# Performance work log

Measured on AMD Instinct MI355X. Metric: run time of the kernel, lower is better.

Reference implementation:

```python
import jax, jax.numpy as jnp
import numpy as np
from jax import lax

# Mamba-2 block, mode='recurrent' (chunked SSD scan), default vanilla causal dwconv
D_MODEL = 2048
D_STATE = 64
D_CONV = 4
HEADDIM = 64
EXPAND = 2
NGROUPS = 1
CHUNK = 64
D_INNER = EXPAND * D_MODEL          # 4096
NHEADS = D_INNER // HEADDIM          # 64
CONV_DIM = D_INNER + 2 * NGROUPS * D_STATE   # 4224
D_IN_PROJ = 2 * D_INNER + 2 * NGROUPS * D_STATE + NHEADS  # 8384
BATCH, SEQ = 2, 4096
EPS = 1e-5


def setup_inputs() -> dict:
    key = jax.random.key(0)
    ks = jax.random.split(key, 8)
    x = jax.random.normal(ks[0], (BATCH, SEQ, D_MODEL), jnp.float32)
    in_proj_w = jax.random.normal(ks[1], (D_IN_PROJ, D_MODEL), jnp.float32) / np.sqrt(D_MODEL)
    conv_w = jax.random.normal(ks[2], (CONV_DIM, D_CONV), jnp.float32) / np.sqrt(D_CONV)
    conv_b = jnp.zeros((CONV_DIM,), jnp.float32)
    # dt_bias = inverse-softplus of dt sampled log-uniform in [1e-3, 1e-1]
    dt = jnp.exp(jax.random.uniform(ks[3], (NHEADS,)) * (np.log(0.1) - np.log(0.001)) + np.log(0.001))
    dt_bias = dt + jnp.log(-jnp.expm1(-dt))
    A_log = jnp.log(jax.random.uniform(ks[4], (NHEADS,), minval=1.0, maxval=16.0))
    D = jnp.ones((NHEADS,), jnp.float32)
    norm_w = jnp.ones((D_INNER,), jnp.float32)
    out_proj_w = jax.random.normal(ks[5], (D_MODEL, D_INNER), jnp.float32) / np.sqrt(D_INNER)
    return dict(x=x, in_proj_w=in_proj_w, conv_w=conv_w, conv_b=conv_b,
                dt_bias=dt_bias, A_log=A_log, D=D, norm_w=norm_w, out_proj_w=out_proj_w)


def _segsum(a):
    """a: (..., T) -> (..., T, T) lower-triangular segment sums."""
    T = a.shape[-1]
    cs = jnp.cumsum(a, axis=-1)
    d = cs[..., :, None] - cs[..., None, :]
    mask = jnp.tril(jnp.ones((T, T), dtype=bool))
    return jnp.where(mask, d, -jnp.inf)


def _forward(x, in_proj_w, conv_w, conv_b, dt_bias, A_log, D, norm_w, out_proj_w):
    Bsz, L, _ = x.shape
    nc = L // CHUNK
    zxbcdt = x @ in_proj_w.T                      # (B,L,D_IN_PROJ)
    z = zxbcdt[..., :D_INNER]
    xBC = zxbcdt[..., D_INNER:D_INNER + CONV_DIM]
    dt = zxbcdt[..., D_INNER + CONV_DIM:]         # (B,L,H)

    # causal depthwise conv1d (padding = d_conv-1, sliced to L) + SiLU
    xBC_t = jnp.transpose(xBC, (0, 2, 1))         # (B,C,L)
    y = lax.conv_general_dilated(xBC_t, conv_w[:, None, :], window_strides=(1,),
                                 padding=[(D_CONV - 1, 0)],
                                 feature_group_count=CONV_DIM,
                                 dimension_numbers=('NCH', 'OIH', 'NCH'))
    y = y + conv_b[None, :, None]
    xBC = jax.nn.silu(jnp.transpose(y, (0, 2, 1)))  # (B,L,C)

    xs = xBC[..., :D_INNER]
    Bm = xBC[..., D_INNER:D_INNER + NGROUPS * D_STATE]
    Cm = xBC[..., D_INNER + NGROUPS * D_STATE:]

    dt = jax.nn.softplus(dt + dt_bias)            # (B,L,H)
    A = -jnp.exp(A_log)                           # (H,)
    dA = dt * A                                   # (B,L,H)

    xh = xs.reshape(Bsz, L, NHEADS, HEADDIM)
    Bh = jnp.repeat(Bm.reshape(Bsz, L, NGROUPS, D_STATE), NHEADS // NGROUPS, axis=2)  # (B,L,H,N)
    Ch = jnp.repeat(Cm.reshape(Bsz, L, NGROUPS, D_STATE), NHEADS // NGROUPS, axis=2)
    xdt = xh * dt[..., None]                      # (B,L,H,P)

    # chunk
    Ac = dA.reshape(Bsz, nc, CHUNK, NHEADS).transpose(0, 1, 3, 2)  # (B,c,H,l)
    A_cumsum = jnp.cumsum(Ac, axis=-1)                             # (B,c,H,l)
    Lmat = jnp.exp(_segsum(Ac))                                    # (B,c,H,l,s)
    Cc = Ch.reshape(Bsz, nc, CHUNK, NHEADS, D_STATE)
    Bc = Bh.reshape(Bsz, nc, CHUNK, NHEADS, D_STATE)
    xc = xdt.reshape(Bsz, nc, CHUNK, NHEADS, HEADDIM)

    # intra-chunk (diagonal blocks)
    Y_diag = jnp.einsum('bclhn,bcshn,bchls,bcshp->bclhp', Cc, Bc, Lmat, xc)

    # per-chunk end states
    decay_states = jnp.exp(A_cumsum[..., -1:] - A_cumsum)          # (B,c,H,l)
    states = jnp.einsum('bcshn,bchs,bcshp->bchpn', Bc, decay_states, xc)  # (B,c,H,P,N)
    chunk_decay = jnp.exp(A_cumsum[..., -1])                       # (B,c,H)

    # inter-chunk recurrence over chunks
    def scan_fn(h, inp):
        dec, st = inp                              # (B,H), (B,H,P,N)
        prev = h
        h = dec[..., None, None] * h + st
        return h, prev

    h0 = jnp.zeros((Bsz, NHEADS, HEADDIM, D_STATE), x.dtype)
    _, prev_states = lax.scan(scan_fn, h0,
                              (chunk_decay.transpose(1, 0, 2), states.transpose(1, 0, 2, 3, 4)))
    prev_states = prev_states.transpose(1, 0, 2, 3, 4)             # (B,c,H,P,N)

    Y_off = jnp.einsum('bclhn,bchpn,bchl->bclhp', Cc, prev_states, jnp.exp(A_cumsum))

    Y = (Y_diag + Y_off).reshape(Bsz, L, NHEADS, HEADDIM) + D[:, None] * xh
    yf = Y.reshape(Bsz, L, D_INNER)

    # gated RMSNorm, then out projection
    yf = yf * jax.nn.silu(z)
    yf = yf * lax.rsqrt(jnp.mean(yf * yf, axis=-1, keepdims=True) + EPS) * norm_w
    return yf @ out_proj_w.T


def reference(x, in_proj_w, conv_w, conv_b, dt_bias, A_log, D, norm_w, out_proj_w):
    return _forward(x, in_proj_w, conv_w, conv_b, dt_bias, A_log, D, norm_w, out_proj_w)
```

## Files before the change

kernel.cpp:

```cpp
#include <hip/hip_runtime.h>

#define BATCH 2
#define SEQ 4096
#define DMODEL 2048
#define DINNER 4096
#define NHEADS 64
#define HEADDIM 64
#define DSTATE 64
#define CONVDIM 4224
#define DINPROJ 8384
#define NCHUNK 64
#define CHUNKL 64
#define MROWS (BATCH*SEQ)

typedef __bf16 bf16_t;
typedef bf16_t bf16x8 __attribute__((ext_vector_type(8)));
typedef float f32x4 __attribute__((ext_vector_type(4)));
typedef unsigned short u16;
typedef u16 u16x8 __attribute__((ext_vector_type(8)));

__device__ __forceinline__ u16 f2bf(float f) {
  unsigned int u = __float_as_uint(f);
  u += 0x7fff + ((u >> 16) & 1);
  return (u16)(u >> 16);
}
__device__ __forceinline__ float bf2f(u16 s) {
  return __uint_as_float(((unsigned int)s) << 16);
}

__device__ __forceinline__ void async_load16(const void* g, void* l) {
  __builtin_amdgcn_global_load_lds(
      (const __attribute__((address_space(1))) void*)g,
      (__attribute__((address_space(3))) void*)l, 16, 0, 0);
}

__global__ __launch_bounds__(256) void cvt_kernel(const float* __restrict__ in,
                                                  u16* __restrict__ out, int n4) {
  int i = blockIdx.x * 256 + threadIdx.x;
  if (i >= n4) return;
  float4 v = *(const float4*)(in + (size_t)i * 4);
  ushort4 o;
  o.x = f2bf(v.x); o.y = f2bf(v.y); o.z = f2bf(v.z); o.w = f2bf(v.w);
  *(ushort4*)(out + (size_t)i * 4) = o;
}

template <int EPI>
__global__ __launch_bounds__(512, 2) void gemm_bt(const u16* __restrict__ A,
                                                  const u16* __restrict__ B,
                                                  int M, int N, int K,
                                                  float* __restrict__ outf,
                                                  u16* __restrict__ z_out,
                                                  u16* __restrict__ xe_out,
                                                  float* __restrict__ bce_out,
                                                  float* __restrict__ dt_out) {
  __shared__ char smem[147456];
  const int tid = threadIdx.x;
  const int w = tid >> 6, lane = tid & 63;
  const int id = blockIdx.y * gridDim.x + blockIdx.x;
  int m0, n0;
  if (EPI == 0) {
    n0 = (id & 7) * 256;
    m0 = (id >> 3) * 128;
  } else {
    const int xcd = id & 7;
    const int q = id >> 3;
    m0 = (xcd * 8 + (q & 7)) * 128;
    n0 = (q >> 3) * 256;
  }
  const int wr = (w >> 2) * 64, wc = (w & 3) * 64;
  const int fr = lane & 15, fq = lane >> 4;
  const int nkt = K >> 6;

  const u16* aptr[2];
  const u16* bptr[4];
#pragma unroll
  for (int p = 0; p < 2; ++p) {
    int d = p * 8192 + tid * 16;
    int row = d >> 7;
    int colb = (d & 127) ^ ((row & 7) << 4);
    aptr[p] = A + (size_t)(m0 + row) * K + (colb >> 1);
  }
#pragma unroll
  for (int p = 0; p < 4; ++p) {
    int d = p * 8192 + tid * 16;
    int row = d >> 7;
    int colb = (d & 127) ^ ((row & 7) << 4);
    int gn = n0 + row;
    if (gn > N - 1) gn = N - 1;
    bptr[p] = B + (size_t)gn * K + (colb >> 1);
  }

  auto stage_to = [&](int bi) {
    char* base = (char*)smem + bi * 49152;
#pragma unroll
    for (int p = 0; p < 2; ++p) {
      async_load16(aptr[p], base + p * 8192 + tid * 16);
      aptr[p] += 64;
    }
#pragma unroll
    for (int p = 0; p < 4; ++p) {
      async_load16(bptr[p], base + 16384 + p * 8192 + tid * 16);
      bptr[p] += 64;
    }
  };

  auto load_frags = [&](int bi, int ks, bf16x8* af, bf16x8* bf) {
    const char* base = (const char*)smem + bi * 49152;
#pragma unroll
    for (int i = 0; i < 4; ++i) {
      int rowa = wr + i * 16 + fr;
      af[i] = *(const bf16x8*)(base + ((rowa * 128 + ks * 64 + fq * 16) ^ ((fr & 7) << 4)));
      int rowb = wc + i * 16 + fr;
      bf[i] = *(const bf16x8*)(base + 16384 +
                               ((rowb * 128 + ks * 64 + fq * 16) ^ ((fr & 7) << 4)));
    }
  };

  f32x4 acc[4][4];
#pragma unroll
  for (int i = 0; i < 4; ++i)
#pragma unroll
    for (int j = 0; j < 4; ++j) acc[i][j] = (f32x4){0.f, 0.f, 0.f, 0.f};

  stage_to(0);
  stage_to(1);
  asm volatile("s_waitcnt vmcnt(6)" ::: "memory");
  __builtin_amdgcn_s_barrier();

  bf16x8 a0[4], b0[4], a1[4], b1[4];
  load_frags(0, 0, a0, b0);

  int cur = 0;
  for (int t = 0; t < nkt; ++t) {
    int nx = cur + 1; if (nx == 3) nx = 0;
    int st = nx + 1; if (st == 3) st = 0;
    load_frags(cur, 1, a1, b1);
    const bool do_stage = (t + 2 < nkt);
    if (do_stage) stage_to(st);
    __builtin_amdgcn_s_setprio(1);
#pragma unroll
    for (int i = 0; i < 4; ++i)
#pragma unroll
      for (int j = 0; j < 4; ++j)
        acc[i][j] = __builtin_amdgcn_mfma_f32_16x16x32_bf16(a0[i], b0[j], acc[i][j], 0, 0, 0);
    __builtin_amdgcn_s_setprio(0);
    if (do_stage) {
      asm volatile("s_waitcnt vmcnt(6)" ::: "memory");
    } else {
      asm volatile("s_waitcnt vmcnt(0)" ::: "memory");
    }
    __builtin_amdgcn_s_barrier();
    if (t + 1 < nkt) load_frags(nx, 0, a0, b0);
    __builtin_amdgcn_s_setprio(1);
#pragma unroll
    for (int i = 0; i < 4; ++i)
#pragma unroll
      for (int j = 0; j < 4; ++j)
        acc[i][j] = __builtin_amdgcn_mfma_f32_16x16x32_bf16(a1[i], b1[j], acc[i][j], 0, 0, 0);
    __builtin_amdgcn_s_setprio(0);
    cur = nx;
  }

#pragma unroll
  for (int i = 0; i < 4; ++i) {
#pragma unroll
    for (int j = 0; j < 4; ++j) {
#pragma unroll
      for (int rr2 = 0; rr2 < 4; ++rr2) {
        int row = m0 + wr + i * 16 + fq * 4 + rr2;
        int col = n0 + wc + j * 16 + fr;
        float v = acc[i][j][rr2];
        if (EPI == 0) {
          if (col < N) outf[(size_t)row * N + col] = v;
        } else {
          if (col < DINNER) {
            z_out[(size_t)row * DINNER + col] = f2bf(v);
          } else if (col < 2 * DINNER) {
            xe_out[(size_t)row * DINNER + (col - DINNER)] = f2bf(v);
          } else if (col < DINNER + CONVDIM) {
            bce_out[(size_t)row * 128 + (col - 2 * DINNER)] = v;
          } else if (col < DINPROJ) {
            dt_out[(size_t)row * NHEADS + (col - DINNER - CONVDIM)] = v;
          }
        }
      }
    }
  }
}

__global__ __launch_bounds__(64) void dt_acs_kernel(float* __restrict__ dt,
                                                    const float* __restrict__ dt_bias,
                                                    const float* __restrict__ A_log,
                                                    float* __restrict__ Acs) {
  const int bid = blockIdx.x;
  const int h = threadIdx.x;
  const float bias = dt_bias[h];
  const float nA = -expf(A_log[h]);
  float run = 0.f;
  float* acs_row = Acs + ((size_t)bid * 64 + h) * 64;
  for (int s = 0; s < 64; ++s) {
    size_t g = ((size_t)bid * 64 + s) * 64 + h;
    float xv = dt[g] + bias;
    float sp = (xv > 20.f) ? xv : log1pf(expf(xv));
    dt[g] = sp;
    run += nA * sp;
    acs_row[s] = run;
  }
}

__global__ __launch_bounds__(256) void conv_silu_kernel(const u16* __restrict__ xe,
                                                        const float* __restrict__ bce,
                                                        const float* __restrict__ conv_w,
                                                        const float* __restrict__ conv_b,
                                                        u16* __restrict__ xs,
                                                        float* __restrict__ Bf,
                                                        float* __restrict__ Cf) {
  const int ch8 = blockIdx.x * 256 + threadIdx.x;
  if (ch8 >= CONVDIM / 8) return;
  const int b = blockIdx.z;
  const int l0 = blockIdx.y * 32;
  const int ch0 = ch8 * 8;
  const bool isx = ch0 < DINNER;
  float w[8][4], cb[8];
#pragma unroll
  for (int j = 0; j < 8; ++j) {
    cb[j] = conv_b[ch0 + j];
#pragma unroll
    for (int t = 0; t < 4; ++t) w[j][t] = conv_w[(ch0 + j) * 4 + t];
  }
  float win[3][8];
#pragma unroll
  for (int t = 0; t < 3; ++t) {
    int l = l0 - 3 + t;
    if (l < 0) {
#pragma unroll
      for (int j = 0; j < 8; ++j) win[t][j] = 0.f;
    } else if (isx) {
      const u16* p = &xe[((size_t)b * SEQ + l) * DINNER + ch0];
      ushort4 a = *(const ushort4*)p, bq = *(const ushort4*)(p + 4);
      win[t][0] = bf2f(a.x); win[t][1] = bf2f(a.y); win[t][2] = bf2f(a.z); win[t][3] = bf2f(a.w);
      win[t][4] = bf2f(bq.x); win[t][5] = bf2f(bq.y); win[t][6] = bf2f(bq.z); win[t][7] = bf2f(bq.w);
    } else {
      const float* p = &bce[((size_t)b * SEQ + l) * 128 + (ch0 - DINNER)];
      float4 a = *(const float4*)p, bq = *(const float4*)(p + 4);
      win[t][0] = a.x; win[t][1] = a.y; win[t][2] = a.z; win[t][3] = a.w;
      win[t][4] = bq.x; win[t][5] = bq.y; win[t][6] = bq.z; win[t][7] = bq.w;
    }
  }
  for (int li = 0; li < 32; ++li) {
    const int l = l0 + li;
    float cur[8];
    if (isx) {
      const u16* p = &xe[((size_t)b * SEQ + l) * DINNER + ch0];
      ushort4 a = *(const ushort4*)p, bq = *(const ushort4*)(p + 4);
      cur[0] = bf2f(a.x); cur[1] = bf2f(a.y); cur[2] = bf2f(a.z); cur[3] = bf2f(a.w);
      cur[4] = bf2f(bq.x); cur[5] = bf2f(bq.y); cur[6] = bf2f(bq.z); cur[7] = bf2f(bq.w);
    } else {
      const float* p = &bce[((size_t)b * SEQ + l) * 128 + (ch0 - DINNER)];
      float4 a = *(const float4*)p, bq = *(const float4*)(p + 4);
      cur[0] = a.x; cur[1] = a.y; cur[2] = a.z; cur[3] = a.w;
      cur[4] = bq.x; cur[5] = bq.y; cur[6] = bq.z; cur[7] = bq.w;
    }
    float o[8];
#pragma unroll
    for (int j = 0; j < 8; ++j) {
      float acc = cb[j] + w[j][0] * win[0][j] + w[j][1] * win[1][j] +
                  w[j][2] * win[2][j] + w[j][3] * cur[j];
      o[j] = acc / (1.f + expf(-acc));
    }
    if (isx) {
      const int h = ch0 >> 6, p0 = ch0 & 63;
      u16* dst = &xs[(((size_t)b * NHEADS + h) * SEQ + l) * 64 + p0];
      ushort4 s0, s1;
      s0.x = f2bf(o[0]); s0.y = f2bf(o[1]); s0.z = f2bf(o[2]); s0.w = f2bf(o[3]);
      s1.x = f2bf(o[4]); s1.y = f2bf(o[5]); s1.z = f2bf(o[6]); s1.w = f2bf(o[7]);
      *(ushort4*)dst = s0;
      *(ushort4*)(dst + 4) = s1;
    } else {
      const int c0 = ch0 - DINNER;
      float* dst = (c0 < DSTATE) ? &Bf[((size_t)b * SEQ + l) * 64 + c0]
                                 : &Cf[((size_t)b * SEQ + l) * 64 + (c0 - DSTATE)];
      float4 f0 = {o[0], o[1], o[2], o[3]}, f1 = {o[4], o[5], o[6], o[7]};
      *(float4*)dst = f0;
      *(float4*)(dst + 4) = f1;
    }
#pragma unroll
    for (int j = 0; j < 8; ++j) { win[0][j] = win[1][j]; win[1][j] = win[2][j]; win[2][j] = cur[j]; }
  }
}

__global__ __launch_bounds__(256) void states_kernel(const u16* __restrict__ xs,
                                                     const float* __restrict__ Bf,
                                                     const float* __restrict__ Acs,
                                                     const float* __restrict__ dtp,
                                                     u16* __restrict__ states) {
  const int bid = blockIdx.x;
  const int h = bid & 63, cc = (bid >> 6) & 63, b = bid >> 12;
  __shared__ char lds[16384 + 256];
  char* Axb = lds;
  char* Bb = lds + 8192;
  float* scale_s = (float*)(lds + 16384);
  const int tid = threadIdx.x;
  const float* acs = Acs + (size_t)bid * 64;
  const size_t blbase = (size_t)b * SEQ + cc * 64;
  if (tid < 64) {
    float alast = acs[63];
    scale_s[tid] = expf(alast - acs[tid]) * dtp[(blbase + tid) * 64 + h];
  }
  __syncthreads();
  const int r = tid >> 2, c0 = (tid & 3) * 16;
  {
    const float sc = scale_s[r];
    const u16* src = &xs[(((size_t)b * NHEADS + h) * SEQ + cc * 64 + r) * 64 + c0];
    u16x8 x0 = *(const u16x8*)src, x1 = *(const u16x8*)(src + 8);
    const float* bsrc = &Bf[(blbase + r) * 64 + c0];
    float4 bv0 = *(const float4*)bsrc, bv1 = *(const float4*)(bsrc + 4);
    float4 bv2 = *(const float4*)(bsrc + 8), bv3 = *(const float4*)(bsrc + 12);
    float ba[16] = {bv0.x, bv0.y, bv0.z, bv0.w, bv1.x, bv1.y, bv1.z, bv1.w,
                    bv2.x, bv2.y, bv2.z, bv2.w, bv3.x, bv3.y, bv3.z, bv3.w};
#pragma unroll
    for (int k = 0; k < 16; ++k) {
      u16 xv = (k < 8) ? x0[k] : x1[k - 8];
      int p = c0 + k;
      *(u16*)(Axb + ((p * 128 + r * 2) ^ ((p & 7) << 4))) = f2bf(bf2f(xv) * sc);
      *(u16*)(Bb + ((p * 128 + r * 2) ^ ((p & 7) << 4))) = f2bf(ba[k]);
    }
  }
  __syncthreads();
  const int w = tid >> 6, lane = tid & 63;
  const int fr = lane & 15, fq = lane >> 4;
  const int pw = w * 16;
  auto ldf = [&](const char* base, int row, int ks) -> bf16x8 {
    return *(const bf16x8*)(base + ((row * 128 + ks * 64 + fq * 16) ^ ((row & 7) << 4)));
  };
  bf16x8 aA[2];
  aA[0] = ldf(Axb, pw + fr, 0);
  aA[1] = ldf(Axb, pw + fr, 1);
  f32x4 acc[4];
#pragma unroll
  for (int j = 0; j < 4; ++j) acc[j] = (f32x4){0.f, 0.f, 0.f, 0.f};
#pragma unroll
  for (int j = 0; j < 4; ++j)
#pragma unroll
    for (int ks = 0; ks < 2; ++ks)
      acc[j] = __builtin_amdgcn_mfma_f32_16x16x32_bf16(aA[ks], ldf(Bb, j * 16 + fr, ks), acc[j], 0, 0, 0);
  u16* so = states + (size_t)bid * 4096;
#pragma unroll
  for (int j = 0; j < 4; ++j)
#pragma unroll
    for (int reg = 0; reg < 4; ++reg)
      so[(pw + fq * 4 + reg) * 64 + j * 16 + fr] = f2bf(acc[j][reg]);
}

__global__ __launch_bounds__(256) void scan_kernel(u16* __restrict__ states,
                                                   const float* __restrict__ Acs) {
  int idx = blockIdx.x * 256 + threadIdx.x;
  int n = idx & 63, p = (idx >> 6) & 63, h = (idx >> 12) & 63, b = idx >> 18;
  float prev = 0.f;
  for (int c = 0; c < 64; ++c) {
    size_t bid = (size_t)(b * 64 + c) * 64 + h;
    size_t off = bid * 4096 + p * 64 + n;
    float sv = bf2f(states[off]);
    float cd = expf(Acs[bid * 64 + 63]);
    states[off] = f2bf(prev);
    prev = cd * prev + sv;
  }
}

__global__ __launch_bounds__(256) void cbt_kernel(const float* __restrict__ Bf,
                                                  const float* __restrict__ Cf,
                                                  float* __restrict__ cbt) {
  const int bc = blockIdx.x;
  __shared__ float Ct[64 * 65];
  __shared__ float Bt[64 * 65];
  const int tid = threadIdx.x;
  const size_t blbase = (size_t)(bc >> 6) * SEQ + (bc & 63) * 64;
  const int c4 = (tid & 15) * 4;
  for (int rr = tid >> 4; rr < 64; rr += 16) {
    float4 cv = *(const float4*)&Cf[(blbase + rr) * 64 + c4];
    float4 bv = *(const float4*)&Bf[(blbase + rr) * 64 + c4];
    Ct[rr * 65 + c4 + 0] = cv.x; Ct[rr * 65 + c4 + 1] = cv.y;
    Ct[rr * 65 + c4 + 2] = cv.z; Ct[rr * 65 + c4 + 3] = cv.w;
    Bt[rr * 65 + c4 + 0] = bv.x; Bt[rr * 65 + c4 + 1] = bv.y;
    Bt[rr * 65 + c4 + 2] = bv.z; Bt[rr * 65 + c4 + 3] = bv.w;
  }
  __syncthreads();
  const int l0 = (tid >> 4) * 4, s0 = (tid & 15) * 4;
  float a1[4][4] = {};
  for (int n = 0; n < 64; ++n) {
    float cv[4], bv[4];
#pragma unroll
    for (int i = 0; i < 4; ++i) { cv[i] = Ct[(l0 + i) * 65 + n]; bv[i] = Bt[(s0 + i) * 65 + n]; }
#pragma unroll
    for (int i = 0; i < 4; ++i)
#pragma unroll
      for (int j = 0; j < 4; ++j) a1[i][j] += cv[i] * bv[j];
  }
  float* dst = cbt + (size_t)bc * 4096;
#pragma unroll
  for (int i = 0; i < 4; ++i) {
    float4 o = {a1[i][0], a1[i][1], a1[i][2], a1[i][3]};
    *(float4*)&dst[(l0 + i) * 64 + s0] = o;
  }
}

__global__ __launch_bounds__(256) void y_kernel(const u16* __restrict__ xs,
                                                const float* __restrict__ cbt,
                                                const float* __restrict__ Cf,
                                                const float* __restrict__ Acs,
                                                const float* __restrict__ dtp,
                                                const u16* __restrict__ prev,
                                                const float* __restrict__ Dv,
                                                u16* __restrict__ zY) {
  const int bid = blockIdx.x;
  const int h = bid & 63, cc = (bid >> 6) & 63, b = bid >> 12;
  const int bc = bid >> 6;
  __shared__ char lds[32768 + 256];
  char* Cb = lds;
  char* Pb = lds + 8192;
  char* Sb = lds + 16384;
  char* Xb = lds + 24576;
  float* acsl = (float*)(lds + 32768);
  const int tid = threadIdx.x;
  const size_t blbase = (size_t)b * SEQ + cc * 64;
  if (tid < 64) acsl[tid] = Acs[(size_t)bid * 64 + tid];

  const int r = tid >> 2, c0 = (tid & 3) * 16;
  {
    const float* src = &Cf[(blbase + r) * 64 + c0];
    float4 a = *(const float4*)src, bq = *(const float4*)(src + 4);
    float4 c2 = *(const float4*)(src + 8), d2 = *(const float4*)(src + 12);
    u16x8 v0 = {f2bf(a.x), f2bf(a.y), f2bf(a.z), f2bf(a.w),
                f2bf(bq.x), f2bf(bq.y), f2bf(bq.z), f2bf(bq.w)};
    u16x8 v1 = {f2bf(c2.x), f2bf(c2.y), f2bf(c2.z), f2bf(c2.w),
                f2bf(d2.x), f2bf(d2.y), f2bf(d2.z), f2bf(d2.w)};
    *(u16x8*)(Cb + ((r * 128 + c0 * 2) ^ ((r & 7) << 4))) = v0;
    *(u16x8*)(Cb + ((r * 128 + c0 * 2 + 16) ^ ((r & 7) << 4))) = v1;
  }
  {
    const u16* src = &prev[(size_t)bid * 4096 + r * 64 + c0];
    u16x8 v0 = *(const u16x8*)src, v1 = *(const u16x8*)(src + 8);
    *(u16x8*)(Pb + ((r * 128 + c0 * 2) ^ ((r & 7) << 4))) = v0;
    *(u16x8*)(Pb + ((r * 128 + c0 * 2 + 16) ^ ((r & 7) << 4))) = v1;
  }
  {
    float dtv = dtp[(blbase + r) * 64 + h];
    const u16* src = &xs[(((size_t)b * NHEADS + h) * SEQ + cc * 64 + r) * 64 + c0];
    u16x8 x0 = *(const u16x8*)src, x1 = *(const u16x8*)(src + 8);
#pragma unroll
    for (int k = 0; k < 16; ++k) {
      u16 xv = (k < 8) ? x0[k] : x1[k - 8];
      u16 o = f2bf(bf2f(xv) * dtv);
      int p = c0 + k;
      *(u16*)(Xb + ((p * 128 + r * 2) ^ ((p & 7) << 4))) = o;
    }
  }
  __syncthreads();
  {
    float al = acsl[r];
    const float* src = &cbt[(size_t)bc * 4096 + r * 64 + c0];
    u16 ov[16];
#pragma unroll
    for (int k = 0; k < 16; ++k) {
      int s = c0 + k;
      float v = (r >= s) ? src[k] * expf(al - acsl[s]) : 0.f;
      ov[k] = f2bf(v);
    }
    u16x8 v0 = {ov[0], ov[1], ov[2], ov[3], ov[4], ov[5], ov[6], ov[7]};
    u16x8 v1 = {ov[8], ov[9], ov[10], ov[11], ov[12], ov[13], ov[14], ov[15]};
    *(u16x8*)(Sb + ((r * 128 + c0 * 2) ^ ((r & 7) << 4))) = v0;
    *(u16x8*)(Sb + ((r * 128 + c0 * 2 + 16) ^ ((r & 7) << 4))) = v1;
  }
  __syncthreads();

  const int w = tid >> 6, lane = tid & 63;
  const int fr = lane & 15, fq = lane >> 4;
  const int lw = w * 16;
  auto ldf = [&](const char* base, int row, int ks) -> bf16x8 {
    return *(const bf16x8*)(base + ((row * 128 + ks * 64 + fq * 16) ^ ((row & 7) << 4)));
  };
  bf16x8 aS[2], aC[2];
#pragma unroll
  for (int ks = 0; ks < 2; ++ks) {
    aS[ks] = ldf(Sb, lw + fr, ks);
    aC[ks] = ldf(Cb, lw + fr, ks);
  }
  f32x4 ay[4], ao[4];
#pragma unroll
  for (int j = 0; j < 4; ++j) { ay[j] = (f32x4){0.f,0.f,0.f,0.f}; ao[j] = (f32x4){0.f,0.f,0.f,0.f}; }
#pragma unroll
  for (int j = 0; j < 4; ++j) {
#pragma unroll
    for (int ks = 0; ks < 2; ++ks) {
      bf16x8 bX = ldf(Xb, j * 16 + fr, ks);
      ay[j] = __builtin_amdgcn_mfma_f32_16x16x32_bf16(aS[ks], bX, ay[j], 0, 0, 0);
      bf16x8 bP = ldf(Pb, j * 16 + fr, ks);
      ao[j] = __builtin_amdgcn_mfma_f32_16x16x32_bf16(aC[ks], bP, ao[j], 0, 0, 0);
    }
  }
  const float Dh = Dv[h];
  float el[4];
#pragma unroll
  for (int reg = 0; reg < 4; ++reg) el[reg] = expf(acsl[lw + fq * 4 + reg]);
#pragma unroll
  for (int j = 0; j < 4; ++j) {
#pragma unroll
    for (int reg = 0; reg < 4; ++reg) {
      int l = lw + fq * 4 + reg, p = j * 16 + fr;
      float yv = ay[j][reg] + el[reg] * ao[j][reg] +
                 Dh * bf2f(xs[(((size_t)b * NHEADS + h) * SEQ + cc * 64 + l) * 64 + p]);
      size_t zoff = (blbase + l) * DINNER + h * 64 + p;
      float zv = bf2f(zY[zoff]);
      zY[zoff] = f2bf(yv * (zv / (1.f + expf(-zv))));
    }
  }
}

__global__ __launch_bounds__(256) void rms_kernel(const u16* __restrict__ Y,
                                                  const float* __restrict__ nw,
                                                  u16* __restrict__ yf) {
  const int row = blockIdx.x, tid = threadIdx.x;
  const u16* yrow = Y + (size_t)row * DINNER;
  float g[16];
  float ss = 0.f;
#pragma unroll
  for (int i = 0; i < 4; ++i) {
    ushort4 yv = *(const ushort4*)&yrow[tid * 16 + i * 4];
    float ya[4] = {bf2f(yv.x), bf2f(yv.y), bf2f(yv.z), bf2f(yv.w)};
#pragma unroll
    for (int j = 0; j < 4; ++j) {
      g[i * 4 + j] = ya[j];
      ss += ya[j] * ya[j];
    }
  }
#pragma unroll
  for (int off = 32; off > 0; off >>= 1) ss += __shfl_down(ss, off, 64);
  __shared__ float red[4];
  if ((tid & 63) == 0) red[tid >> 6] = ss;
  __syncthreads();
  float tot = red[0] + red[1] + red[2] + red[3];
  float sc = rsqrtf(tot * (1.f / (float)DINNER) + 1e-5f);
#pragma unroll
  for (int i = 0; i < 4; ++i) {
    float4 nv = *(const float4*)&nw[tid * 16 + i * 4];
    float na[4] = {nv.x, nv.y, nv.z, nv.w};
    ushort4 o;
    o.x = f2bf(g[i * 4 + 0] * sc * na[0]);
    o.y = f2bf(g[i * 4 + 1] * sc * na[1]);
    o.z = f2bf(g[i * 4 + 2] * sc * na[2]);
    o.w = f2bf(g[i * 4 + 3] * sc * na[3]);
    *(ushort4*)&yf[(size_t)row * DINNER + tid * 16 + i * 4] = o;
  }
}

extern "C" void kernel_launch(void* const* d_in, const int* in_sizes, int n_in,
                              void* d_out, int out_size, void* d_ws, size_t ws_size,
                              hipStream_t stream) {
  const float* x = (const float*)d_in[0];
  const float* in_proj_w = (const float*)d_in[1];
  const float* conv_w = (const float*)d_in[2];
  const float* conv_b = (const float*)d_in[3];
  const float* dt_bias = (const float*)d_in[4];
  const float* A_log = (const float*)d_in[5];
  const float* Dvec = (const float*)d_in[6];
  const float* norm_w = (const float*)d_in[7];
  const float* out_proj_w = (const float*)d_in[8];

  char* ws = (char*)d_ws;
  u16* xbf    = (u16*)(ws + 0);
  u16* winbf  = (u16*)(ws + 33554432);
  u16* xs     = (u16*)(ws + 0);
  u16* yfbf   = (u16*)(ws + 0);
  u16* zY     = (u16*)(ws + 67895296);
  u16* xe     = (u16*)(ws + 135004160);
  u16* statesb= (u16*)(ws + 135004160);
  u16* woutbf = (u16*)(ws + 135004160);
  float* bce  = (float*)(ws + 202113024);
  float* dtb  = (float*)(ws + 206307328);
  float* Acs  = (float*)(ws + 208404480);
  float* Bfb  = (float*)(ws + 210501632);
  float* Cfb  = (float*)(ws + 212598784);
  float* cbt  = (float*)(ws + 214695936);

  cvt_kernel<<<16384, 256, 0, stream>>>(x, xbf, 4194304);
  cvt_kernel<<<16768, 256, 0, stream>>>(in_proj_w, winbf, 4292608);

  gemm_bt<1><<<dim3(64, 33), 512, 0, stream>>>(xbf, winbf, MROWS, DINPROJ, DMODEL,
                                               nullptr, zY, xe, bce, dtb);

  dt_acs_kernel<<<128, 64, 0, stream>>>(dtb, dt_bias, A_log, Acs);

  conv_silu_kernel<<<dim3(3, 128, 2), 256, 0, stream>>>(xe, bce, conv_w, conv_b, xs, Bfb, Cfb);

  states_kernel<<<8192, 256, 0, stream>>>(xs, Bfb, Acs, dtb, statesb);
  scan_kernel<<<2048, 256, 0, stream>>>(statesb, Acs);
  cbt_kernel<<<128, 256, 0, stream>>>(Bfb, Cfb, cbt);
  y_kernel<<<8192, 256, 0, stream>>>(xs, cbt, Cfb, Acs, dtb, statesb, Dvec, zY);

  rms_kernel<<<8192, 256, 0, stream>>>(zY, norm_w, yfbf);

  cvt_kernel<<<8192, 256, 0, stream>>>(out_proj_w, woutbf, 2097152);
  gemm_bt<0><<<dim3(64, 8), 512, 0, stream>>>(yfbf, woutbf, MROWS, DMODEL, DINNER,
                                              (float*)d_out, nullptr, nullptr, nullptr, nullptr);
}
```

Baseline: 744.1 us.

## Fuse RMSNorm into y_kernel partial sums and out-proj GEMM epilogue

The y_kernel now accumulates per-row per-head sums of squares of the gated output and writes them to a partial-sum buffer. A small kernel reduces these into per-row rsqrt scales. The norm weight is folded into the bf16 conversion of out_proj_w, and the row scale is applied in the GEMM epilogue, so the standalone RMSNorm pass over the 64MB activation buffer goes away. The cost is an extra shuffle reduction in y_kernel and slightly different rounding, since the unnormalized bf16 values feed the GEMM directly.

```diff
diff --git a/kernel.cpp b/kernel.cpp
--- a/kernel.cpp
+++ b/kernel.cpp
@@ -44,11 +44,26 @@
   *(ushort4*)(out + (size_t)i * 4) = o;
 }
 
+__global__ __launch_bounds__(256) void cvt_norm_kernel(const float* __restrict__ in,
+                                                       const float* __restrict__ nw,
+                                                       u16* __restrict__ out, int n4) {
+  int i = blockIdx.x * 256 + threadIdx.x;
+  if (i >= n4) return;
+  int k = (i * 4) & (DINNER - 1);
+  float4 v = *(const float4*)(in + (size_t)i * 4);
+  float4 nv = *(const float4*)(nw + k);
+  ushort4 o;
+  o.x = f2bf(v.x * nv.x); o.y = f2bf(v.y * nv.y);
+  o.z = f2bf(v.z * nv.z); o.w = f2bf(v.w * nv.w);
+  *(ushort4*)(out + (size_t)i * 4) = o;
+}
+
 template <int EPI>
 __global__ __launch_bounds__(512, 2) void gemm_bt(const u16* __restrict__ A,
                                                   const u16* __restrict__ B,
                                                   int M, int N, int K,
                                                   float* __restrict__ outf,
+                                                  const float* __restrict__ scrow,
                                                   u16* __restrict__ z_out,
                                                   u16* __restrict__ xe_out,
                                                   float* __restrict__ bce_out,
@@ -171,7 +186,7 @@
         int col = n0 + wc + j * 16 + fr;
         float v = acc[i][j][rr2];
         if (EPI == 0) {
-          if (col < N) outf[(size_t)row * N + col] = v;
+          if (col < N) outf[(size_t)row * N + col] = v * scrow[row];
         } else {
           if (col < DINNER) {
             z_out[(size_t)row * DINNER + col] = f2bf(v);
@@ -411,7 +426,8 @@
                                                 const float* __restrict__ dtp,
                                                 const u16* __restrict__ prev,
                                                 const float* __restrict__ Dv,
-                                                u16* __restrict__ zY) {
+                                                u16* __restrict__ zY,
+                                                float* __restrict__ psum) {
   const int bid = blockIdx.x;
   const int h = bid & 63, cc = (bid >> 6) & 63, b = bid >> 12;
   const int bc = bid >> 6;
@@ -499,7 +515,7 @@
     }
   }
   const float Dh = Dv[h];
-  float el[4];
+  float el[4], rs[4] = {0.f, 0.f, 0.f, 0.f};
 #pragma unroll
   for (int reg = 0; reg < 4; ++reg) el[reg] = expf(acsl[lw + fq * 4 + reg]);
 #pragma unroll
@@ -511,46 +527,32 @@
                  Dh * bf2f(xs[(((size_t)b * NHEADS + h) * SEQ + cc * 64 + l) * 64 + p]);
       size_t zoff = (blbase + l) * DINNER + h * 64 + p;
       float zv = bf2f(zY[zoff]);
-      zY[zoff] = f2bf(yv * (zv / (1.f + expf(-zv))));
-    }
-  }
-}
-
-__global__ __launch_bounds__(256) void rms_kernel(const u16* __restrict__ Y,
-                                                  const float* __restrict__ nw,
-                                                  u16* __restrict__ yf) {
-  const int row = blockIdx.x, tid = threadIdx.x;
-  const u16* yrow = Y + (size_t)row * DINNER;
-  float g[16];
-  float ss = 0.f;
-#pragma unroll
-  for (int i = 0; i < 4; ++i) {
-    ushort4 yv = *(const ushort4*)&yrow[tid * 16 + i * 4];
-    float ya[4] = {bf2f(yv.x), bf2f(yv.y), bf2f(yv.z), bf2f(yv.w)};
-#pragma unroll
-    for (int j = 0; j < 4; ++j) {
-      g[i * 4 + j] = ya[j];
-      ss += ya[j] * ya[j];
-    }
-  }
-#pragma unroll
-  for (int off = 32; off > 0; off >>= 1) ss += __shfl_down(ss, off, 64);
-  __shared__ float red[4];
-  if ((tid & 63) == 0) red[tid >> 6] = ss;
-  __syncthreads();
-  float tot = red[0] + red[1] + red[2] + red[3];
-  float sc = rsqrtf(tot * (1.f / (float)DINNER) + 1e-5f);
-#pragma unroll
-  for (int i = 0; i < 4; ++i) {
-    float4 nv = *(const float4*)&nw[tid * 16 + i * 4];
-    float na[4] = {nv.x, nv.y, nv.z, nv.w};
-    ushort4 o;
-    o.x = f2bf(g[i * 4 + 0] * sc * na[0]);
-    o.y = f2bf(g[i * 4 + 1] * sc * na[1]);
-    o.z = f2bf(g[i * 4 + 2] * sc * na[2]);
-    o.w = f2bf(g[i * 4 + 3] * sc * na[3]);
-    *(ushort4*)&yf[(size_t)row * DINNER + tid * 16 + i * 4] = o;
-  }
+      float g = yv * (zv / (1.f + expf(-zv)));
+      zY[zoff] = f2bf(g);
+      rs[reg] += g * g;
+    }
+  }
+#pragma unroll
+  for (int reg = 0; reg < 4; ++reg) {
+#pragma unroll
+    for (int off = 1; off < 16; off <<= 1) rs[reg] += __shfl_xor(rs[reg], off, 64);
+  }
+  if (fr == 0) {
+#pragma unroll
+    for (int reg = 0; reg < 4; ++reg)
+      psum[(size_t)bid * 64 + lw + fq * 4 + reg] = rs[reg];
+  }
+}
+
+__global__ __launch_bounds__(256) void rms_finish_kernel(const float* __restrict__ psum,
+                                                         float* __restrict__ scrow) {
+  int row = blockIdx.x * 256 + threadIdx.x;
+  int b = row >> 12, cc = (row >> 6) & 63, l = row & 63;
+  const float* p = psum + (((size_t)(b * 64 + cc)) * 64) * 64 + l;
+  float s = 0.f;
+#pragma unroll 8
+  for (int h = 0; h < 64; ++h) s += p[h * 64];
+  scrow[row] = rsqrtf(s * (1.f / (float)DINNER) + 1e-5f);
 }
 
 extern "C" void kernel_launch(void* const* d_in, const int* in_sizes, int n_in,
@@ -570,12 +572,13 @@
   u16* xbf    = (u16*)(ws + 0);
   u16* winbf  = (u16*)(ws + 33554432);
   u16* xs     = (u16*)(ws + 0);
-  u16* yfbf   = (u16*)(ws + 0);
   u16* zY     = (u16*)(ws + 67895296);
   u16* xe     = (u16*)(ws + 135004160);
   u16* statesb= (u16*)(ws + 135004160);
   u16* woutbf = (u16*)(ws + 135004160);
   float* bce  = (float*)(ws + 202113024);
+  float* psum = (float*)(ws + 202113024);
+  float* scrow= (float*)(ws + 204210176);
   float* dtb  = (float*)(ws + 206307328);
   float* Acs  = (float*)(ws + 208404480);
   float* Bfb  = (float*)(ws + 210501632);
@@ -586,7 +589,7 @@
   cvt_kernel<<<16768, 256, 0, stream>>>(in_proj_w, winbf, 4292608);
 
   gemm_bt<1><<<dim3(64, 33), 512, 0, stream>>>(xbf, winbf, MROWS, DINPROJ, DMODEL,
-                                               nullptr, zY, xe, bce, dtb);
+                                               nullptr, nullptr, zY, xe, bce, dtb);
 
   dt_acs_kernel<<<128, 64, 0, stream>>>(dtb, dt_bias, A_log, Acs);
 
@@ -595,11 +598,11 @@
   states_kernel<<<8192, 256, 0, stream>>>(xs, Bfb, Acs, dtb, statesb);
   scan_kernel<<<2048, 256, 0, stream>>>(statesb, Acs);
   cbt_kernel<<<128, 256, 0, stream>>>(Bfb, Cfb, cbt);
-  y_kernel<<<8192, 256, 0, stream>>>(xs, cbt, Cfb, Acs, dtb, statesb, Dvec, zY);
-
-  rms_kernel<<<8192, 256, 0, stream>>>(zY, norm_w, yfbf);
-
-  cvt_kernel<<<8192, 256, 0, stream>>>(out_proj_w, woutbf, 2097152);
-  gemm_bt<0><<<dim3(64, 8), 512, 0, stream>>>(yfbf, woutbf, MROWS, DMODEL, DINNER,
-                                              (float*)d_out, nullptr, nullptr, nullptr, nullptr);
-}
+  y_kernel<<<8192, 256, 0, stream>>>(xs, cbt, Cfb, Acs, dtb, statesb, Dvec, zY, psum);
+
+  rms_finish_kernel<<<32, 256, 0, stream>>>(psum, scrow);
+
+  cvt_norm_kernel<<<8192, 256, 0, stream>>>(out_proj_w, norm_w, woutbf, 2097152);
+  gemm_bt<0><<<dim3(64, 8), 512, 0, stream>>>(zY, woutbf, MROWS, DMODEL, DINNER,
+                                              (float*)d_out, scrow, nullptr, nullptr, nullptr, nullptr);
+}
```

Result: no change. 732.4 us (-1.6%).
